# Optimization experiments

Hardware: AMD Instinct MI355X
Metric: run time of the kernel (lower is better)

## Reference

```python
import jax, jax.numpy as jnp
import numpy as np

N_NODES = 100000
N_EDGES = 3200000
NFEAT = 128
NHID = 128


def gcn_conv(x, edge_index, W, b):
    """PyG-style GCNConv: out = D^{-1/2} (A + I) D^{-1/2} (x @ W) + b."""
    n = x.shape[0]
    loop = jnp.arange(n, dtype=edge_index.dtype)
    src = jnp.concatenate([edge_index[0], loop])  # [E + N]
    dst = jnp.concatenate([edge_index[1], loop])  # [E + N]
    # symmetric normalization (degree counted at target, self-loops included)
    deg = jax.ops.segment_sum(jnp.ones_like(dst, dtype=x.dtype), dst, num_segments=n)
    dinv = jnp.where(deg > 0, jax.lax.rsqrt(jnp.maximum(deg, 1.0)), 0.0)
    norm = dinv[src] * dinv[dst]  # [E + N]
    h = x @ W  # [N, F_out] dense projection before aggregation (PyG order)
    msg = h[src] * norm[:, None]  # irregular gather, [E + N, F_out]
    out = jax.ops.segment_sum(msg, dst, num_segments=n)  # scatter-add
    return out + b


def setup_inputs() -> dict:
    key = jax.random.key(0)
    k1, k2, k3, k4 = jax.random.split(key, 4)
    x = jax.random.normal(k1, (N_NODES, NFEAT), dtype=jnp.float32)
    edge_index = jax.random.randint(k2, (2, N_EDGES), 0, N_NODES, dtype=jnp.int64)
    W1 = jax.random.normal(k3, (NFEAT, NHID), dtype=jnp.float32) * 0.05
    b1 = jnp.zeros((NHID,), dtype=jnp.float32)
    W2 = jax.random.normal(k4, (NHID, NHID), dtype=jnp.float32) * 0.05
    b2 = jnp.zeros((NHID,), dtype=jnp.float32)
    return {"x": x, "edge_index": edge_index, "W1": W1, "b1": b1, "W2": W2, "b2": b2}


def reference(x, edge_index, W1, b1, W2, b2):
    # Encoder.forward in eval mode (dropout is identity when training=False)
    h = jax.nn.relu(gcn_conv(x, edge_index, W1, b1))
    h = jax.nn.relu(gcn_conv(h, edge_index, W2, b2))
    return h
```

## Files before the change

kernel.cpp:

```cpp
#include <hip/hip_runtime.h>
#include <hip/hip_fp16.h>
#include <math.h>


#define MB (1u << 20)
#define BCAP 5120
#define EBLK 512

typedef _Float16 f16x8 __attribute__((ext_vector_type(8)));
typedef float f32x4 __attribute__((ext_vector_type(4)));

__global__ __launch_bounds__(256) void k_append(const int* __restrict__ src,
                                                const int* __restrict__ dst,
                                                int* __restrict__ bcnt,
                                                int* __restrict__ staging,
                                                const float* __restrict__ W1,
                                                const float* __restrict__ W2,
                                                _Float16* __restrict__ Wt1,
                                                _Float16* __restrict__ Wt2,
                                                int E, int N, int B) {
  if (blockIdx.x >= EBLK) {
    int idx = (blockIdx.x - EBLK) * 256 + threadIdx.x;
    const float* W = (idx < 16384) ? W1 : W2;
    _Float16* Wt = (idx < 16384) ? Wt1 : Wt2;
    int i = idx & 16383;
    int k = i >> 7, n = i & 127;
    Wt[n * 128 + k] = (_Float16)W[k * 128 + n];
    return;
  }
  __shared__ int lh[1024];
  __shared__ int lb[1024];
  const int t = threadIdx.x;
  const int per = (E + EBLK - 1) / EBLK;
  const int e0 = blockIdx.x * per;
  const int e1 = min(e0 + per, E);

  for (int i = t; i < B; i += 256) lh[i] = 0;
  __syncthreads();
  for (int e = e0 + t; e < e1; e += 256) {
    int d = dst[e], s = src[e];
    if ((unsigned)d < (unsigned)N && (unsigned)s < (unsigned)N)
      atomicAdd(&lh[d >> 7], 1);
  }
  __syncthreads();
  for (int i = t; i < B; i += 256) {
    int c = lh[i];
    lb[i] = c ? atomicAdd(&bcnt[i], c) : 0;
  }
  __syncthreads();
  for (int i = t; i < B; i += 256) lh[i] = 0;
  __syncthreads();
  for (int e = e0 + t; e < e1; e += 256) {
    int d = dst[e], s = src[e];
    if ((unsigned)d < (unsigned)N && (unsigned)s < (unsigned)N) {
      int b = d >> 7;
      int lp = atomicAdd(&lh[b], 1);
      int pos = lb[b] + lp;
      if (pos < BCAP)
        staging[(size_t)b * BCAP + pos] = ((d & 127) << 25) | s;
    }
  }
}

__global__ __launch_bounds__(256) void k_build(const int* __restrict__ staging,
                                               const int* __restrict__ bcnt,
                                               int* __restrict__ rowptr,
                                               float* __restrict__ dinv,
                                               int* __restrict__ col, int N, int B) {
  __shared__ int red[256];
  __shared__ int cnts[128];
  __shared__ int off[128];
  __shared__ int cur[128];
  const int b = blockIdx.x;
  const int t = threadIdx.x;
  const int cnt = min(bcnt[b], BCAP);
  const int* stg = staging + (size_t)b * BCAP;

  int partial = 0;
  for (int i = t; i < b; i += 256) partial += min(bcnt[i], BCAP);
  red[t] = partial;
  if (t < 128) cnts[t] = 0;
  __syncthreads();
  #pragma unroll
  for (int o = 128; o > 0; o >>= 1) {
    if (t < o) red[t] += red[t + o];
    __syncthreads();
  }
  const int ebase = red[0];

  for (int i = t; i < cnt; i += 256)
    atomicAdd(&cnts[((unsigned)stg[i]) >> 25], 1);
  __syncthreads();
  if (t < 128) off[t] = cnts[t];
  __syncthreads();
  for (int d = 1; d < 128; d <<= 1) {
    int v = 0;
    if (t < 128 && t >= d) v = off[t - d];
    __syncthreads();
    if (t < 128) off[t] += v;
    __syncthreads();
  }
  if (t < 128) {
    int node = b * 128 + t;
    if (node < N) {
      int ex = off[t] - cnts[t];
      rowptr[node] = ebase + ex;
      cur[t] = ex;
      dinv[node] = rsqrtf((float)(cnts[t] + 1));
    }
  }
  if (b == B - 1 && t == 0) rowptr[N] = ebase + cnt;
  __syncthreads();
  for (int i = t; i < cnt; i += 256) {
    int p = stg[i];
    int dl = ((unsigned)p) >> 25;
    int s = p & 0x1FFFFFF;
    int lp = atomicAdd(&cur[dl], 1);
    col[ebase + lp] = s;
  }
}

__device__ __forceinline__ void load8(const float* X, size_t base, int kg,
                                      bool relu, _Float16* tmp) {
  float4 v0 = *reinterpret_cast<const float4*>(X + base + kg * 8);
  float4 v1 = *reinterpret_cast<const float4*>(X + base + kg * 8 + 4);
  if (relu) {
    v0.x = fmaxf(v0.x, 0.f); v0.y = fmaxf(v0.y, 0.f);
    v0.z = fmaxf(v0.z, 0.f); v0.w = fmaxf(v0.w, 0.f);
    v1.x = fmaxf(v1.x, 0.f); v1.y = fmaxf(v1.y, 0.f);
    v1.z = fmaxf(v1.z, 0.f); v1.w = fmaxf(v1.w, 0.f);
  }
  tmp[0] = (_Float16)v0.x; tmp[1] = (_Float16)v0.y;
  tmp[2] = (_Float16)v0.z; tmp[3] = (_Float16)v0.w;
  tmp[4] = (_Float16)v1.x; tmp[5] = (_Float16)v1.y;
  tmp[6] = (_Float16)v1.z; tmp[7] = (_Float16)v1.w;
}
__device__ __forceinline__ void load8(const __half* X, size_t base, int kg,
                                      bool relu, _Float16* tmp) {
  uint4 u = *reinterpret_cast<const uint4*>(X + base + kg * 8);
  const _Float16* p = reinterpret_cast<const _Float16*>(&u);
  #pragma unroll
  for (int j = 0; j < 8; j++) {
    _Float16 f = p[j];
    if (relu && (float)f < 0.f) f = (_Float16)0.f;
    tmp[j] = f;
  }
}

template <bool RELU_IN, typename InT>
__global__ __launch_bounds__(256) void k_gemm(const InT* __restrict__ X,
                                              const _Float16* __restrict__ Wt,
                                              const float* __restrict__ dinv,
                                              __half* __restrict__ H, int M) {
  __shared__ __align__(16) _Float16 Xs[64 * 128];
  __shared__ __align__(16) _Float16 Ws[128 * 128];
  const int rb = blockIdx.x * 64;
  const int t = threadIdx.x;

  for (int idx = t; idx < 1024; idx += 256) {
    int row = idx >> 4, kg = idx & 15;
    int grow = rb + row;
    _Float16 tmp[8];
    if (grow < M) {
      load8(X, (size_t)grow * 128, kg, RELU_IN, tmp);
    } else {
      #pragma unroll
      for (int j = 0; j < 8; j++) tmp[j] = (_Float16)0.f;
    }
    int g = kg ^ (row & 7);
    *reinterpret_cast<uint4*>(&Xs[row * 128 + g * 8]) = *reinterpret_cast<uint4*>(tmp);
  }
  for (int idx = t; idx < 2048; idx += 256) {
    int n = idx >> 4, kg = idx & 15;
    uint4 v = *reinterpret_cast<const uint4*>(Wt + n * 128 + kg * 8);
    int g = kg ^ (n & 7);
    *reinterpret_cast<uint4*>(&Ws[n * 128 + g * 8]) = v;
  }
  __syncthreads();

  const int wid = t >> 6;
  const int l = t & 63;
  const int lrow = wid * 16 + (l & 15);
  const int kq = l >> 4;

  f16x8 afrag[4];
  #pragma unroll
  for (int kc = 0; kc < 4; kc++) {
    int kg = kc * 4 + kq;
    int g = kg ^ (lrow & 7);
    afrag[kc] = *reinterpret_cast<const f16x8*>(&Xs[lrow * 128 + g * 8]);
  }
  float dv[4];
  #pragma unroll
  for (int i = 0; i < 4; i++) {
    int grow = rb + wid * 16 + kq * 4 + i;
    dv[i] = (grow < M) ? dinv[grow] : 0.f;
  }

  #pragma unroll 2
  for (int nt = 0; nt < 8; nt++) {
    const int n = nt * 16 + (l & 15);
    f32x4 acc = {};
    #pragma unroll
    for (int kc = 0; kc < 4; kc++) {
      int kg = kc * 4 + kq;
      int g = kg ^ (n & 7);
      f16x8 bfrag = *reinterpret_cast<const f16x8*>(&Ws[n * 128 + g * 8]);
      acc = __builtin_amdgcn_mfma_f32_16x16x32_f16(afrag[kc], bfrag, acc, 0, 0, 0);
    }
    #pragma unroll
    for (int i = 0; i < 4; i++) {
      int grow = rb + wid * 16 + kq * 4 + i;
      if (grow < M)
        H[(size_t)grow * 128 + nt * 16 + (l & 15)] = __float2half(acc[i] * dv[i]);
    }
  }
}

template <bool RELU_OUT, typename OutT>
__global__ __launch_bounds__(256) void k_pull(const __half* __restrict__ hs,
                                              const int* __restrict__ rowptr,
                                              const int* __restrict__ col,
                                              const float* __restrict__ dinv,
                                              const float* __restrict__ bias,
                                              OutT* __restrict__ out, int N) {
  int node = blockIdx.x * 4 + (threadIdx.x >> 6);
  if (node >= N) return;
  node = __builtin_amdgcn_readfirstlane(node);
  const int lane = threadIdx.x & 63;
  const int half = lane >> 5;
  const int fo = (lane & 31) << 2;
  const int start = __builtin_amdgcn_readfirstlane(rowptr[node]);
  const int cnt = __builtin_amdgcn_readfirstlane(rowptr[node + 1]) - start;

  float4 a0 = make_float4(0.f, 0.f, 0.f, 0.f);
  float4 a1 = a0, a2 = a0, a3 = a0;

#define GATHER(sidx, dstacc)                                                   \
  {                                                                            \
    const __half2* p_ =                                                        \
        reinterpret_cast<const __half2*>(hs + (size_t)(sidx) * 128 + fo);      \
    float2 f0_ = __half22float2(p_[0]);                                        \
    float2 f1_ = __half22float2(p_[1]);                                        \
    dstacc.x += f0_.x; dstacc.y += f0_.y;                                      \
    dstacc.z += f1_.x; dstacc.w += f1_.y;                                      \
  }

  int k = 0;
  for (; k + 8 <= cnt; k += 8) {
    int s0 = col[start + k + 0 + half];
    int s1 = col[start + k + 2 + half];
    int s2 = col[start + k + 4 + half];
    int s3 = col[start + k + 6 + half];
    GATHER(s0, a0);
    GATHER(s1, a1);
    GATHER(s2, a2);
    GATHER(s3, a3);
  }
  for (; k + 2 <= cnt; k += 2) {
    int s = col[start + k + half];
    GATHER(s, a0);
  }
  if (k < cnt) {
    int s = col[start + k];
    if (!half) {
      GATHER(s, a1);
    }
  }
#undef GATHER

  float4 acc;
  acc.x = (a0.x + a1.x) + (a2.x + a3.x);
  acc.y = (a0.y + a1.y) + (a2.y + a3.y);
  acc.z = (a0.z + a1.z) + (a2.z + a3.z);
  acc.w = (a0.w + a1.w) + (a2.w + a3.w);
  acc.x += __shfl_xor(acc.x, 32, 64);
  acc.y += __shfl_xor(acc.y, 32, 64);
  acc.z += __shfl_xor(acc.z, 32, 64);
  acc.w += __shfl_xor(acc.w, 32, 64);

  if (!half) {
    const __half2* sp = reinterpret_cast<const __half2*>(hs + (size_t)node * 128 + fo);
    float2 s0 = __half22float2(sp[0]);
    float2 s1 = __half22float2(sp[1]);
    float di = dinv[node];
    float4 bv = *reinterpret_cast<const float4*>(bias + fo);
    float4 o;
    o.x = fmaf(di, acc.x + s0.x, bv.x);
    o.y = fmaf(di, acc.y + s0.y, bv.y);
    o.z = fmaf(di, acc.z + s1.x, bv.z);
    o.w = fmaf(di, acc.w + s1.y, bv.w);
    if (RELU_OUT) {
      o.x = fmaxf(o.x, 0.f); o.y = fmaxf(o.y, 0.f);
      o.z = fmaxf(o.z, 0.f); o.w = fmaxf(o.w, 0.f);
    }
    if constexpr (sizeof(OutT) == 2) {
      __half2 p0 = __float22half2_rn(make_float2(o.x, o.y));
      __half2 p1 = __float22half2_rn(make_float2(o.z, o.w));
      __half2* op = reinterpret_cast<__half2*>((__half*)out + (size_t)node * 128 + fo);
      op[0] = p0;
      op[1] = p1;
    } else {
      *reinterpret_cast<float4*>((float*)out + (size_t)node * 128 + fo) = o;
    }
  }
}

extern "C" void kernel_launch(void* const* d_in, const int* in_sizes, int n_in,
                              void* d_out, int out_size, void* d_ws, size_t ws_size,
                              hipStream_t stream) {
  const float* x  = (const float*)d_in[0];
  const int*   ei = (const int*)d_in[1];
  const float* W1 = (const float*)d_in[2];
  const float* b1 = (const float*)d_in[3];
  const float* W2 = (const float*)d_in[4];
  const float* b2 = (const float*)d_in[5];
  float* out = (float*)d_out;

  const int N = in_sizes[0] / 128;
  const int E = in_sizes[1] / 2;
  const int B = (N + 127) >> 7;
  const int* src = ei;
  const int* dst = ei + E;

  char* ws = (char*)d_ws;
  int*      bcnt    = (int*)     (ws);
  float*    dinv    = (float*)   (ws + 64 * 1024);
  int*      rowptr  = (int*)     (ws + 512 * 1024);
  int*      col     = (int*)     (ws + 1 * MB);
  _Float16* Wt1     = (_Float16*)(ws + 14 * MB - 128 * 1024);
  _Float16* Wt2     = (_Float16*)(ws + 14 * MB - 64 * 1024);
  __half*   h       = (__half*)  (ws + 18 * MB);
  __half*   agg     = (__half*)  (ws + 44 * MB);
  int*      staging = (int*)     (ws + 44 * MB);

  dim3 b256(256);

  hipMemsetAsync(bcnt, 0, (size_t)B * 4, stream);
  k_append<<<EBLK + 128, b256, 0, stream>>>(src, dst, bcnt, staging,
                                            W1, W2, Wt1, Wt2, E, N, B);
  k_build<<<B, b256, 0, stream>>>(staging, bcnt, rowptr, dinv, col, N, B);

  dim3 ggrid((N + 63) / 64);
  dim3 pgrid((N + 3) / 4);

  k_gemm<false, float><<<ggrid, b256, 0, stream>>>(x, Wt1, dinv, h, N);
  k_pull<false, __half><<<pgrid, b256, 0, stream>>>(h, rowptr, col, dinv, b1, agg, N);

  k_gemm<true, __half><<<ggrid, b256, 0, stream>>>(agg, Wt2, dinv, h, N);
  k_pull<true, float><<<pgrid, b256, 0, stream>>>(h, rowptr, col, dinv, b2, out, N);
}
```

Measured before the change: 347.6 us.

## Overlap layer-1 GEMM with edge bucketing and fuse aggregation into layer-2 GEMM

The layer-1 GEMM now writes unscaled features, so it no longer depends on dinv and runs in the same launch as the edge-bucketing blocks. The source-side normalization moves into the gather loop as a per-edge dinv lookup. Layer-1 aggregation, bias and ReLU are fused with the layer-2 GEMM in one 1024-thread kernel, which removes the intermediate agg buffer round trip, the memset and two launches. In exchange, every edge does an extra random dinv load, and the fused kernel makes each wave aggregate four nodes in sequence before the MFMA stage.

```diff
diff --git a/kernel.cpp b/kernel.cpp
--- a/kernel.cpp
+++ b/kernel.cpp
@@ -10,54 +10,133 @@
 typedef _Float16 f16x8 __attribute__((ext_vector_type(8)));
 typedef float f32x4 __attribute__((ext_vector_type(4)));
 
-__global__ __launch_bounds__(256) void k_append(const int* __restrict__ src,
-                                                const int* __restrict__ dst,
-                                                int* __restrict__ bcnt,
-                                                int* __restrict__ staging,
-                                                const float* __restrict__ W1,
-                                                const float* __restrict__ W2,
-                                                _Float16* __restrict__ Wt1,
-                                                _Float16* __restrict__ Wt2,
-                                                int E, int N, int B) {
-  if (blockIdx.x >= EBLK) {
-    int idx = (blockIdx.x - EBLK) * 256 + threadIdx.x;
+__global__ __launch_bounds__(256) void k_init(const float* __restrict__ W1,
+                                              const float* __restrict__ W2,
+                                              _Float16* __restrict__ Wt1,
+                                              _Float16* __restrict__ Wt2,
+                                              int* __restrict__ bcnt, int B) {
+  if (blockIdx.x < 128) {
+    int idx = blockIdx.x * 256 + threadIdx.x;
     const float* W = (idx < 16384) ? W1 : W2;
     _Float16* Wt = (idx < 16384) ? Wt1 : Wt2;
     int i = idx & 16383;
     int k = i >> 7, n = i & 127;
     Wt[n * 128 + k] = (_Float16)W[k * 128 + n];
+  } else {
+    for (int i = threadIdx.x; i < B; i += 256) bcnt[i] = 0;
+  }
+}
+
+union F1Smem {
+  struct { int lh[1024]; int lb[1024]; } a;
+  struct { _Float16 Xs[64 * 128]; _Float16 Ws[128 * 128]; } g;
+};
+
+__global__ __launch_bounds__(256) void k_f1(const float* __restrict__ X,
+                                            const _Float16* __restrict__ Wt1,
+                                            __half* __restrict__ H, int M, int GB,
+                                            const int* __restrict__ src,
+                                            const int* __restrict__ dst,
+                                            int* __restrict__ bcnt,
+                                            int* __restrict__ staging,
+                                            int E, int N, int B) {
+  __shared__ __align__(16) F1Smem sm;
+  const int t = threadIdx.x;
+
+  if ((int)blockIdx.x >= GB) {
+    int* lh = sm.a.lh;
+    int* lb = sm.a.lb;
+    const int bid = blockIdx.x - GB;
+    const int per = (E + EBLK - 1) / EBLK;
+    const int e0 = bid * per;
+    const int e1 = min(e0 + per, E);
+
+    for (int i = t; i < B; i += 256) lh[i] = 0;
+    __syncthreads();
+    for (int e = e0 + t; e < e1; e += 256) {
+      int d = dst[e], s = src[e];
+      if ((unsigned)d < (unsigned)N && (unsigned)s < (unsigned)N)
+        atomicAdd(&lh[d >> 7], 1);
+    }
+    __syncthreads();
+    for (int i = t; i < B; i += 256) {
+      int c = lh[i];
+      lb[i] = c ? atomicAdd(&bcnt[i], c) : 0;
+    }
+    __syncthreads();
+    for (int i = t; i < B; i += 256) lh[i] = 0;
+    __syncthreads();
+    for (int e = e0 + t; e < e1; e += 256) {
+      int d = dst[e], s = src[e];
+      if ((unsigned)d < (unsigned)N && (unsigned)s < (unsigned)N) {
+        int b = d >> 7;
+        int lp = atomicAdd(&lh[b], 1);
+        int pos = lb[b] + lp;
+        if (pos < BCAP)
+          staging[(size_t)b * BCAP + pos] = ((d & 127) << 25) | s;
+      }
+    }
     return;
   }
-  __shared__ int lh[1024];
-  __shared__ int lb[1024];
-  const int t = threadIdx.x;
-  const int per = (E + EBLK - 1) / EBLK;
-  const int e0 = blockIdx.x * per;
-  const int e1 = min(e0 + per, E);
-
-  for (int i = t; i < B; i += 256) lh[i] = 0;
-  __syncthreads();
-  for (int e = e0 + t; e < e1; e += 256) {
-    int d = dst[e], s = src[e];
-    if ((unsigned)d < (unsigned)N && (unsigned)s < (unsigned)N)
-      atomicAdd(&lh[d >> 7], 1);
-  }
-  __syncthreads();
-  for (int i = t; i < B; i += 256) {
-    int c = lh[i];
-    lb[i] = c ? atomicAdd(&bcnt[i], c) : 0;
-  }
-  __syncthreads();
-  for (int i = t; i < B; i += 256) lh[i] = 0;
-  __syncthreads();
-  for (int e = e0 + t; e < e1; e += 256) {
-    int d = dst[e], s = src[e];
-    if ((unsigned)d < (unsigned)N && (unsigned)s < (unsigned)N) {
-      int b = d >> 7;
-      int lp = atomicAdd(&lh[b], 1);
-      int pos = lb[b] + lp;
-      if (pos < BCAP)
-        staging[(size_t)b * BCAP + pos] = ((d & 127) << 25) | s;
+
+  _Float16* Xs = sm.g.Xs;
+  _Float16* Ws = sm.g.Ws;
+  const int rb = blockIdx.x * 64;
+
+  for (int idx = t; idx < 1024; idx += 256) {
+    int row = idx >> 4, kg = idx & 15;
+    int grow = rb + row;
+    _Float16 tmp[8];
+    if (grow < M) {
+      float4 v0 = *reinterpret_cast<const float4*>(X + (size_t)grow * 128 + kg * 8);
+      float4 v1 = *reinterpret_cast<const float4*>(X + (size_t)grow * 128 + kg * 8 + 4);
+      tmp[0] = (_Float16)v0.x; tmp[1] = (_Float16)v0.y;
+      tmp[2] = (_Float16)v0.z; tmp[3] = (_Float16)v0.w;
+      tmp[4] = (_Float16)v1.x; tmp[5] = (_Float16)v1.y;
+      tmp[6] = (_Float16)v1.z; tmp[7] = (_Float16)v1.w;
+    } else {
+      #pragma unroll
+      for (int j = 0; j < 8; j++) tmp[j] = (_Float16)0.f;
+    }
+    int g = kg ^ (row & 7);
+    *reinterpret_cast<uint4*>(&Xs[row * 128 + g * 8]) = *reinterpret_cast<uint4*>(tmp);
+  }
+  for (int idx = t; idx < 2048; idx += 256) {
+    int n = idx >> 4, kg = idx & 15;
+    uint4 v = *reinterpret_cast<const uint4*>(Wt1 + n * 128 + kg * 8);
+    int g = kg ^ (n & 7);
+    *reinterpret_cast<uint4*>(&Ws[n * 128 + g * 8]) = v;
+  }
+  __syncthreads();
+
+  const int wid = t >> 6;
+  const int l = t & 63;
+  const int lrow = wid * 16 + (l & 15);
+  const int kq = l >> 4;
+
+  f16x8 afrag[4];
+  #pragma unroll
+  for (int kc = 0; kc < 4; kc++) {
+    int kg = kc * 4 + kq;
+    int g = kg ^ (lrow & 7);
+    afrag[kc] = *reinterpret_cast<const f16x8*>(&Xs[lrow * 128 + g * 8]);
+  }
+  #pragma unroll 2
+  for (int nt = 0; nt < 8; nt++) {
+    const int n = nt * 16 + (l & 15);
+    f32x4 acc = {};
+    #pragma unroll
+    for (int kc = 0; kc < 4; kc++) {
+      int kg = kc * 4 + kq;
+      int g = kg ^ (n & 7);
+      f16x8 bfrag = *reinterpret_cast<const f16x8*>(&Ws[n * 128 + g * 8]);
+      acc = __builtin_amdgcn_mfma_f32_16x16x32_f16(afrag[kc], bfrag, acc, 0, 0, 0);
+    }
+    #pragma unroll
+    for (int i = 0; i < 4; i++) {
+      int grow = rb + wid * 16 + kq * 4 + i;
+      if (grow < M)
+        H[(size_t)grow * 128 + nt * 16 + (l & 15)] = __float2half(acc[i]);
     }
   }
 }
@@ -120,69 +199,83 @@
   }
 }
 
-__device__ __forceinline__ void load8(const float* X, size_t base, int kg,
-                                      bool relu, _Float16* tmp) {
-  float4 v0 = *reinterpret_cast<const float4*>(X + base + kg * 8);
-  float4 v1 = *reinterpret_cast<const float4*>(X + base + kg * 8 + 4);
-  if (relu) {
-    v0.x = fmaxf(v0.x, 0.f); v0.y = fmaxf(v0.y, 0.f);
-    v0.z = fmaxf(v0.z, 0.f); v0.w = fmaxf(v0.w, 0.f);
-    v1.x = fmaxf(v1.x, 0.f); v1.y = fmaxf(v1.y, 0.f);
-    v1.z = fmaxf(v1.z, 0.f); v1.w = fmaxf(v1.w, 0.f);
-  }
-  tmp[0] = (_Float16)v0.x; tmp[1] = (_Float16)v0.y;
-  tmp[2] = (_Float16)v0.z; tmp[3] = (_Float16)v0.w;
-  tmp[4] = (_Float16)v1.x; tmp[5] = (_Float16)v1.y;
-  tmp[6] = (_Float16)v1.z; tmp[7] = (_Float16)v1.w;
-}
-__device__ __forceinline__ void load8(const __half* X, size_t base, int kg,
-                                      bool relu, _Float16* tmp) {
-  uint4 u = *reinterpret_cast<const uint4*>(X + base + kg * 8);
-  const _Float16* p = reinterpret_cast<const _Float16*>(&u);
-  #pragma unroll
-  for (int j = 0; j < 8; j++) {
-    _Float16 f = p[j];
-    if (relu && (float)f < 0.f) f = (_Float16)0.f;
-    tmp[j] = f;
-  }
-}
-
-template <bool RELU_IN, typename InT>
-__global__ __launch_bounds__(256) void k_gemm(const InT* __restrict__ X,
-                                              const _Float16* __restrict__ Wt,
-                                              const float* __restrict__ dinv,
-                                              __half* __restrict__ H, int M) {
+__device__ __forceinline__ float2 gather_row_sum(const __half* __restrict__ hs,
+                                                 const int* __restrict__ col,
+                                                 const float* __restrict__ dinv,
+                                                 int start, int cnt, int lane) {
+  const __half2* h2 = reinterpret_cast<const __half2*>(hs);
+  float ax0 = 0.f, ay0 = 0.f, ax1 = 0.f, ay1 = 0.f;
+  float ax2 = 0.f, ay2 = 0.f, ax3 = 0.f, ay3 = 0.f;
+  int k = 0;
+  for (; k + 4 <= cnt; k += 4) {
+    int s0 = col[start + k + 0];
+    int s1 = col[start + k + 1];
+    int s2 = col[start + k + 2];
+    int s3 = col[start + k + 3];
+    float d0 = dinv[s0], d1 = dinv[s1], d2 = dinv[s2], d3 = dinv[s3];
+    float2 v0 = __half22float2(h2[(size_t)s0 * 64 + lane]);
+    float2 v1 = __half22float2(h2[(size_t)s1 * 64 + lane]);
+    float2 v2 = __half22float2(h2[(size_t)s2 * 64 + lane]);
+    float2 v3 = __half22float2(h2[(size_t)s3 * 64 + lane]);
+    ax0 = fmaf(v0.x, d0, ax0); ay0 = fmaf(v0.y, d0, ay0);
+    ax1 = fmaf(v1.x, d1, ax1); ay1 = fmaf(v1.y, d1, ay1);
+    ax2 = fmaf(v2.x, d2, ax2); ay2 = fmaf(v2.y, d2, ay2);
+    ax3 = fmaf(v3.x, d3, ax3); ay3 = fmaf(v3.y, d3, ay3);
+  }
+  for (; k < cnt; k++) {
+    int s = col[start + k];
+    float d = dinv[s];
+    float2 v = __half22float2(h2[(size_t)s * 64 + lane]);
+    ax0 = fmaf(v.x, d, ax0); ay0 = fmaf(v.y, d, ay0);
+  }
+  return make_float2((ax0 + ax1) + (ax2 + ax3), (ay0 + ay1) + (ay2 + ay3));
+}
+
+__global__ __launch_bounds__(1024) void k_pullgemm(const __half* __restrict__ hs,
+                                                   const int* __restrict__ rowptr,
+                                                   const int* __restrict__ col,
+                                                   const float* __restrict__ dinv,
+                                                   const float* __restrict__ b1,
+                                                   const _Float16* __restrict__ Wt2,
+                                                   __half* __restrict__ H2, int N) {
   __shared__ __align__(16) _Float16 Xs[64 * 128];
   __shared__ __align__(16) _Float16 Ws[128 * 128];
-  const int rb = blockIdx.x * 64;
   const int t = threadIdx.x;
-
-  for (int idx = t; idx < 1024; idx += 256) {
-    int row = idx >> 4, kg = idx & 15;
-    int grow = rb + row;
-    _Float16 tmp[8];
-    if (grow < M) {
-      load8(X, (size_t)grow * 128, kg, RELU_IN, tmp);
-    } else {
-      #pragma unroll
-      for (int j = 0; j < 8; j++) tmp[j] = (_Float16)0.f;
-    }
-    int g = kg ^ (row & 7);
-    *reinterpret_cast<uint4*>(&Xs[row * 128 + g * 8]) = *reinterpret_cast<uint4*>(tmp);
-  }
-  for (int idx = t; idx < 2048; idx += 256) {
+  const int nb = blockIdx.x * 64;
+
+  for (int idx = t; idx < 2048; idx += 1024) {
     int n = idx >> 4, kg = idx & 15;
-    uint4 v = *reinterpret_cast<const uint4*>(Wt + n * 128 + kg * 8);
+    uint4 v = *reinterpret_cast<const uint4*>(Wt2 + n * 128 + kg * 8);
     int g = kg ^ (n & 7);
     *reinterpret_cast<uint4*>(&Ws[n * 128 + g * 8]) = v;
   }
-  __syncthreads();
-
-  const int wid = t >> 6;
-  const int l = t & 63;
-  const int lrow = wid * 16 + (l & 15);
-  const int kq = l >> 4;
-
+
+  const int w = t >> 6, lane = t & 63;
+  const __half2* h2 = reinterpret_cast<const __half2*>(hs);
+
+  for (int rep = 0; rep < 4; rep++) {
+    const int r = w * 4 + rep;
+    const int node = nb + r;
+    float2 o = make_float2(0.f, 0.f);
+    if (node < N) {
+      const int start = __builtin_amdgcn_readfirstlane(rowptr[node]);
+      const int cnt = __builtin_amdgcn_readfirstlane(rowptr[node + 1]) - start;
+      float2 acc = gather_row_sum(hs, col, dinv, start, cnt, lane);
+      float di = dinv[node];
+      float2 self = __half22float2(h2[(size_t)node * 64 + lane]);
+      float2 bv = reinterpret_cast<const float2*>(b1)[lane];
+      o.x = fmaxf(fmaf(di, fmaf(self.x, di, acc.x), bv.x), 0.f);
+      o.y = fmaxf(fmaf(di, fmaf(self.y, di, acc.y), bv.y), 0.f);
+    }
+    int kg = lane >> 2;
+    int off = (lane & 3) * 2;
+    __half2 oh = __float22half2_rn(o);
+    *reinterpret_cast<__half2*>(&Xs[r * 128 + (kg ^ (r & 7)) * 8 + off]) = oh;
+  }
+  __syncthreads();
+
+  const int lrow = (w & 3) * 16 + (lane & 15);
+  const int kq = lane >> 4;
   f16x8 afrag[4];
   #pragma unroll
   for (int kc = 0; kc < 4; kc++) {
@@ -190,16 +283,10 @@
     int g = kg ^ (lrow & 7);
     afrag[kc] = *reinterpret_cast<const f16x8*>(&Xs[lrow * 128 + g * 8]);
   }
-  float dv[4];
   #pragma unroll
-  for (int i = 0; i < 4; i++) {
-    int grow = rb + wid * 16 + kq * 4 + i;
-    dv[i] = (grow < M) ? dinv[grow] : 0.f;
-  }
-
-  #pragma unroll 2
-  for (int nt = 0; nt < 8; nt++) {
-    const int n = nt * 16 + (l & 15);
+  for (int q = 0; q < 2; q++) {
+    int nt = (w >> 2) * 2 + q;
+    int n = nt * 16 + (lane & 15);
     f32x4 acc = {};
     #pragma unroll
     for (int kc = 0; kc < 4; kc++) {
@@ -210,100 +297,34 @@
     }
     #pragma unroll
     for (int i = 0; i < 4; i++) {
-      int grow = rb + wid * 16 + kq * 4 + i;
-      if (grow < M)
-        H[(size_t)grow * 128 + nt * 16 + (l & 15)] = __float2half(acc[i] * dv[i]);
-    }
-  }
-}
-
-template <bool RELU_OUT, typename OutT>
-__global__ __launch_bounds__(256) void k_pull(const __half* __restrict__ hs,
-                                              const int* __restrict__ rowptr,
-                                              const int* __restrict__ col,
-                                              const float* __restrict__ dinv,
-                                              const float* __restrict__ bias,
-                                              OutT* __restrict__ out, int N) {
+      int grow = nb + (w & 3) * 16 + kq * 4 + i;
+      if (grow < N)
+        H2[(size_t)grow * 128 + nt * 16 + (lane & 15)] = __float2half(acc[i]);
+    }
+  }
+}
+
+__global__ __launch_bounds__(256) void k_pull2(const __half* __restrict__ hs,
+                                               const int* __restrict__ rowptr,
+                                               const int* __restrict__ col,
+                                               const float* __restrict__ dinv,
+                                               const float* __restrict__ bias,
+                                               float* __restrict__ out, int N) {
   int node = blockIdx.x * 4 + (threadIdx.x >> 6);
   if (node >= N) return;
   node = __builtin_amdgcn_readfirstlane(node);
   const int lane = threadIdx.x & 63;
-  const int half = lane >> 5;
-  const int fo = (lane & 31) << 2;
   const int start = __builtin_amdgcn_readfirstlane(rowptr[node]);
   const int cnt = __builtin_amdgcn_readfirstlane(rowptr[node + 1]) - start;
-
-  float4 a0 = make_float4(0.f, 0.f, 0.f, 0.f);
-  float4 a1 = a0, a2 = a0, a3 = a0;
-
-#define GATHER(sidx, dstacc)                                                   \
-  {                                                                            \
-    const __half2* p_ =                                                        \
-        reinterpret_cast<const __half2*>(hs + (size_t)(sidx) * 128 + fo);      \
-    float2 f0_ = __half22float2(p_[0]);                                        \
-    float2 f1_ = __half22float2(p_[1]);                                        \
-    dstacc.x += f0_.x; dstacc.y += f0_.y;                                      \
-    dstacc.z += f1_.x; dstacc.w += f1_.y;                                      \
-  }
-
-  int k = 0;
-  for (; k + 8 <= cnt; k += 8) {
-    int s0 = col[start + k + 0 + half];
-    int s1 = col[start + k + 2 + half];
-    int s2 = col[start + k + 4 + half];
-    int s3 = col[start + k + 6 + half];
-    GATHER(s0, a0);
-    GATHER(s1, a1);
-    GATHER(s2, a2);
-    GATHER(s3, a3);
-  }
-  for (; k + 2 <= cnt; k += 2) {
-    int s = col[start + k + half];
-    GATHER(s, a0);
-  }
-  if (k < cnt) {
-    int s = col[start + k];
-    if (!half) {
-      GATHER(s, a1);
-    }
-  }
-#undef GATHER
-
-  float4 acc;
-  acc.x = (a0.x + a1.x) + (a2.x + a3.x);
-  acc.y = (a0.y + a1.y) + (a2.y + a3.y);
-  acc.z = (a0.z + a1.z) + (a2.z + a3.z);
-  acc.w = (a0.w + a1.w) + (a2.w + a3.w);
-  acc.x += __shfl_xor(acc.x, 32, 64);
-  acc.y += __shfl_xor(acc.y, 32, 64);
-  acc.z += __shfl_xor(acc.z, 32, 64);
-  acc.w += __shfl_xor(acc.w, 32, 64);
-
-  if (!half) {
-    const __half2* sp = reinterpret_cast<const __half2*>(hs + (size_t)node * 128 + fo);
-    float2 s0 = __half22float2(sp[0]);
-    float2 s1 = __half22float2(sp[1]);
-    float di = dinv[node];
-    float4 bv = *reinterpret_cast<const float4*>(bias + fo);
-    float4 o;
-    o.x = fmaf(di, acc.x + s0.x, bv.x);
-    o.y = fmaf(di, acc.y + s0.y, bv.y);
-    o.z = fmaf(di, acc.z + s1.x, bv.z);
-    o.w = fmaf(di, acc.w + s1.y, bv.w);
-    if (RELU_OUT) {
-      o.x = fmaxf(o.x, 0.f); o.y = fmaxf(o.y, 0.f);
-      o.z = fmaxf(o.z, 0.f); o.w = fmaxf(o.w, 0.f);
-    }
-    if constexpr (sizeof(OutT) == 2) {
-      __half2 p0 = __float22half2_rn(make_float2(o.x, o.y));
-      __half2 p1 = __float22half2_rn(make_float2(o.z, o.w));
-      __half2* op = reinterpret_cast<__half2*>((__half*)out + (size_t)node * 128 + fo);
-      op[0] = p0;
-      op[1] = p1;
-    } else {
-      *reinterpret_cast<float4*>((float*)out + (size_t)node * 128 + fo) = o;
-    }
-  }
+  float2 acc = gather_row_sum(hs, col, dinv, start, cnt, lane);
+  float di = dinv[node];
+  float2 self = __half22float2(
+      reinterpret_cast<const __half2*>(hs)[(size_t)node * 64 + lane]);
+  float2 bv = reinterpret_cast<const float2*>(bias)[lane];
+  float2 o;
+  o.x = fmaxf(fmaf(di, fmaf(self.x, di, acc.x), bv.x), 0.f);
+  o.y = fmaxf(fmaf(di, fmaf(self.y, di, acc.y), bv.y), 0.f);
+  reinterpret_cast<float2*>(out)[(size_t)node * 64 + lane] = o;
 }
 
 extern "C" void kernel_launch(void* const* d_in, const int* in_sizes, int n_in,
@@ -320,6 +341,7 @@
   const int N = in_sizes[0] / 128;
   const int E = in_sizes[1] / 2;
   const int B = (N + 127) >> 7;
+  const int GB = (N + 63) / 64;
   const int* src = ei;
   const int* dst = ei + E;
 
@@ -331,22 +353,15 @@
   _Float16* Wt1     = (_Float16*)(ws + 14 * MB - 128 * 1024);
   _Float16* Wt2     = (_Float16*)(ws + 14 * MB - 64 * 1024);
   __half*   h       = (__half*)  (ws + 18 * MB);
-  __half*   agg     = (__half*)  (ws + 44 * MB);
   int*      staging = (int*)     (ws + 44 * MB);
+  __half*   h2      = (__half*)  (ws + 44 * MB);
 
   dim3 b256(256);
 
-  hipMemsetAsync(bcnt, 0, (size_t)B * 4, stream);
-  k_append<<<EBLK + 128, b256, 0, stream>>>(src, dst, bcnt, staging,
-                                            W1, W2, Wt1, Wt2, E, N, B);
+  k_init<<<129, b256, 0, stream>>>(W1, W2, Wt1, Wt2, bcnt, B);
+  k_f1<<<GB + EBLK, b256, 0, stream>>>(x, Wt1, h, N, GB, src, dst, bcnt,
+                                       staging, E, N, B);
   k_build<<<B, b256, 0, stream>>>(staging, bcnt, rowptr, dinv, col, N, B);
-
-  dim3 ggrid((N + 63) / 64);
-  dim3 pgrid((N + 3) / 4);
-
-  k_gemm<false, float><<<ggrid, b256, 0, stream>>>(x, Wt1, dinv, h, N);
-  k_pull<false, __half><<<pgrid, b256, 0, stream>>>(h, rowptr, col, dinv, b1, agg, N);
-
-  k_gemm<true, __half><<<ggrid, b256, 0, stream>>>(agg, Wt2, dinv, h, N);
-  k_pull<true, float><<<pgrid, b256, 0, stream>>>(h, rowptr, col, dinv, b2, out, N);
-}
+  k_pullgemm<<<GB, dim3(1024), 0, stream>>>(h, rowptr, col, dinv, b1, Wt2, h2, N);
+  k_pull2<<<(N + 3) / 4, b256, 0, stream>>>(h2, rowptr, col, dinv, b2, out, N);
+}
```

New measurement: 353.7 us. Within noise of the previous version (+1.8%).

## Fuse first GEMM with edge bucketing and move source normalization into gather

Applied to the files above, without the earlier changes.

The first projection X@W1 no longer depends on the degree normalization, because dinv[src] is now applied per edge inside the gather. That lets the GEMM run in the same launch as the edge-bucketing blocks, so the dense work overlaps the atomic-heavy append phase. The memset and weight transpose move into a small init kernel, and the ReLU on the layer-1 output moves into the pull epilogue, which removes it from the second GEMM's load. The cost is an extra dinv load per gathered edge, and the staging area no longer aliases agg, so the workspace layout changes.

```diff
diff --git a/kernel.cpp b/kernel.cpp
--- a/kernel.cpp
+++ b/kernel.cpp
@@ -10,54 +10,133 @@
 typedef _Float16 f16x8 __attribute__((ext_vector_type(8)));
 typedef float f32x4 __attribute__((ext_vector_type(4)));
 
-__global__ __launch_bounds__(256) void k_append(const int* __restrict__ src,
-                                                const int* __restrict__ dst,
-                                                int* __restrict__ bcnt,
-                                                int* __restrict__ staging,
-                                                const float* __restrict__ W1,
-                                                const float* __restrict__ W2,
-                                                _Float16* __restrict__ Wt1,
-                                                _Float16* __restrict__ Wt2,
-                                                int E, int N, int B) {
-  if (blockIdx.x >= EBLK) {
-    int idx = (blockIdx.x - EBLK) * 256 + threadIdx.x;
+__global__ __launch_bounds__(256) void k_init(const float* __restrict__ W1,
+                                              const float* __restrict__ W2,
+                                              _Float16* __restrict__ Wt1,
+                                              _Float16* __restrict__ Wt2,
+                                              int* __restrict__ bcnt, int B) {
+  if (blockIdx.x < 128) {
+    int idx = blockIdx.x * 256 + threadIdx.x;
     const float* W = (idx < 16384) ? W1 : W2;
     _Float16* Wt = (idx < 16384) ? Wt1 : Wt2;
     int i = idx & 16383;
     int k = i >> 7, n = i & 127;
     Wt[n * 128 + k] = (_Float16)W[k * 128 + n];
+  } else {
+    for (int i = threadIdx.x; i < B; i += 256) bcnt[i] = 0;
+  }
+}
+
+union F1Smem {
+  struct { int lh[1024]; int lb[1024]; } a;
+  struct { _Float16 Xs[64 * 128]; _Float16 Ws[128 * 128]; } g;
+};
+
+__global__ __launch_bounds__(256) void k_f1(const float* __restrict__ X,
+                                            const _Float16* __restrict__ Wt1,
+                                            __half* __restrict__ H, int M, int GB,
+                                            const int* __restrict__ src,
+                                            const int* __restrict__ dst,
+                                            int* __restrict__ bcnt,
+                                            int* __restrict__ staging,
+                                            int E, int N, int B) {
+  __shared__ __align__(16) F1Smem sm;
+  const int t = threadIdx.x;
+
+  if ((int)blockIdx.x >= GB) {
+    int* lh = sm.a.lh;
+    int* lb = sm.a.lb;
+    const int bid = blockIdx.x - GB;
+    const int per = (E + EBLK - 1) / EBLK;
+    const int e0 = bid * per;
+    const int e1 = min(e0 + per, E);
+
+    for (int i = t; i < B; i += 256) lh[i] = 0;
+    __syncthreads();
+    for (int e = e0 + t; e < e1; e += 256) {
+      int d = dst[e], s = src[e];
+      if ((unsigned)d < (unsigned)N && (unsigned)s < (unsigned)N)
+        atomicAdd(&lh[d >> 7], 1);
+    }
+    __syncthreads();
+    for (int i = t; i < B; i += 256) {
+      int c = lh[i];
+      lb[i] = c ? atomicAdd(&bcnt[i], c) : 0;
+    }
+    __syncthreads();
+    for (int i = t; i < B; i += 256) lh[i] = 0;
+    __syncthreads();
+    for (int e = e0 + t; e < e1; e += 256) {
+      int d = dst[e], s = src[e];
+      if ((unsigned)d < (unsigned)N && (unsigned)s < (unsigned)N) {
+        int b = d >> 7;
+        int lp = atomicAdd(&lh[b], 1);
+        int pos = lb[b] + lp;
+        if (pos < BCAP)
+          staging[(size_t)b * BCAP + pos] = ((d & 127) << 25) | s;
+      }
+    }
     return;
   }
-  __shared__ int lh[1024];
-  __shared__ int lb[1024];
-  const int t = threadIdx.x;
-  const int per = (E + EBLK - 1) / EBLK;
-  const int e0 = blockIdx.x * per;
-  const int e1 = min(e0 + per, E);
-
-  for (int i = t; i < B; i += 256) lh[i] = 0;
-  __syncthreads();
-  for (int e = e0 + t; e < e1; e += 256) {
-    int d = dst[e], s = src[e];
-    if ((unsigned)d < (unsigned)N && (unsigned)s < (unsigned)N)
-      atomicAdd(&lh[d >> 7], 1);
-  }
-  __syncthreads();
-  for (int i = t; i < B; i += 256) {
-    int c = lh[i];
-    lb[i] = c ? atomicAdd(&bcnt[i], c) : 0;
-  }
-  __syncthreads();
-  for (int i = t; i < B; i += 256) lh[i] = 0;
-  __syncthreads();
-  for (int e = e0 + t; e < e1; e += 256) {
-    int d = dst[e], s = src[e];
-    if ((unsigned)d < (unsigned)N && (unsigned)s < (unsigned)N) {
-      int b = d >> 7;
-      int lp = atomicAdd(&lh[b], 1);
-      int pos = lb[b] + lp;
-      if (pos < BCAP)
-        staging[(size_t)b * BCAP + pos] = ((d & 127) << 25) | s;
+
+  _Float16* Xs = sm.g.Xs;
+  _Float16* Ws = sm.g.Ws;
+  const int rb = blockIdx.x * 64;
+
+  for (int idx = t; idx < 1024; idx += 256) {
+    int row = idx >> 4, kg = idx & 15;
+    int grow = rb + row;
+    _Float16 tmp[8];
+    if (grow < M) {
+      float4 v0 = *reinterpret_cast<const float4*>(X + (size_t)grow * 128 + kg * 8);
+      float4 v1 = *reinterpret_cast<const float4*>(X + (size_t)grow * 128 + kg * 8 + 4);
+      tmp[0] = (_Float16)v0.x; tmp[1] = (_Float16)v0.y;
+      tmp[2] = (_Float16)v0.z; tmp[3] = (_Float16)v0.w;
+      tmp[4] = (_Float16)v1.x; tmp[5] = (_Float16)v1.y;
+      tmp[6] = (_Float16)v1.z; tmp[7] = (_Float16)v1.w;
+    } else {
+      #pragma unroll
+      for (int j = 0; j < 8; j++) tmp[j] = (_Float16)0.f;
+    }
+    int g = kg ^ (row & 7);
+    *reinterpret_cast<uint4*>(&Xs[row * 128 + g * 8]) = *reinterpret_cast<uint4*>(tmp);
+  }
+  for (int idx = t; idx < 2048; idx += 256) {
+    int n = idx >> 4, kg = idx & 15;
+    uint4 v = *reinterpret_cast<const uint4*>(Wt1 + n * 128 + kg * 8);
+    int g = kg ^ (n & 7);
+    *reinterpret_cast<uint4*>(&Ws[n * 128 + g * 8]) = v;
+  }
+  __syncthreads();
+
+  const int wid = t >> 6;
+  const int l = t & 63;
+  const int lrow = wid * 16 + (l & 15);
+  const int kq = l >> 4;
+
+  f16x8 afrag[4];
+  #pragma unroll
+  for (int kc = 0; kc < 4; kc++) {
+    int kg = kc * 4 + kq;
+    int g = kg ^ (lrow & 7);
+    afrag[kc] = *reinterpret_cast<const f16x8*>(&Xs[lrow * 128 + g * 8]);
+  }
+  #pragma unroll 2
+  for (int nt = 0; nt < 8; nt++) {
+    const int n = nt * 16 + (l & 15);
+    f32x4 acc = {};
+    #pragma unroll
+    for (int kc = 0; kc < 4; kc++) {
+      int kg = kc * 4 + kq;
+      int g = kg ^ (n & 7);
+      f16x8 bfrag = *reinterpret_cast<const f16x8*>(&Ws[n * 128 + g * 8]);
+      acc = __builtin_amdgcn_mfma_f32_16x16x32_f16(afrag[kc], bfrag, acc, 0, 0, 0);
+    }
+    #pragma unroll
+    for (int i = 0; i < 4; i++) {
+      int grow = rb + wid * 16 + kq * 4 + i;
+      if (grow < M)
+        H[(size_t)grow * 128 + nt * 16 + (l & 15)] = __float2half(acc[i]);
     }
   }
 }
@@ -120,37 +199,8 @@
   }
 }
 
-__device__ __forceinline__ void load8(const float* X, size_t base, int kg,
-                                      bool relu, _Float16* tmp) {
-  float4 v0 = *reinterpret_cast<const float4*>(X + base + kg * 8);
-  float4 v1 = *reinterpret_cast<const float4*>(X + base + kg * 8 + 4);
-  if (relu) {
-    v0.x = fmaxf(v0.x, 0.f); v0.y = fmaxf(v0.y, 0.f);
-    v0.z = fmaxf(v0.z, 0.f); v0.w = fmaxf(v0.w, 0.f);
-    v1.x = fmaxf(v1.x, 0.f); v1.y = fmaxf(v1.y, 0.f);
-    v1.z = fmaxf(v1.z, 0.f); v1.w = fmaxf(v1.w, 0.f);
-  }
-  tmp[0] = (_Float16)v0.x; tmp[1] = (_Float16)v0.y;
-  tmp[2] = (_Float16)v0.z; tmp[3] = (_Float16)v0.w;
-  tmp[4] = (_Float16)v1.x; tmp[5] = (_Float16)v1.y;
-  tmp[6] = (_Float16)v1.z; tmp[7] = (_Float16)v1.w;
-}
-__device__ __forceinline__ void load8(const __half* X, size_t base, int kg,
-                                      bool relu, _Float16* tmp) {
-  uint4 u = *reinterpret_cast<const uint4*>(X + base + kg * 8);
-  const _Float16* p = reinterpret_cast<const _Float16*>(&u);
-  #pragma unroll
-  for (int j = 0; j < 8; j++) {
-    _Float16 f = p[j];
-    if (relu && (float)f < 0.f) f = (_Float16)0.f;
-    tmp[j] = f;
-  }
-}
-
-template <bool RELU_IN, typename InT>
-__global__ __launch_bounds__(256) void k_gemm(const InT* __restrict__ X,
+__global__ __launch_bounds__(256) void k_gemm(const __half* __restrict__ X,
                                               const _Float16* __restrict__ Wt,
-                                              const float* __restrict__ dinv,
                                               __half* __restrict__ H, int M) {
   __shared__ __align__(16) _Float16 Xs[64 * 128];
   __shared__ __align__(16) _Float16 Ws[128 * 128];
@@ -160,15 +210,11 @@
   for (int idx = t; idx < 1024; idx += 256) {
     int row = idx >> 4, kg = idx & 15;
     int grow = rb + row;
-    _Float16 tmp[8];
-    if (grow < M) {
-      load8(X, (size_t)grow * 128, kg, RELU_IN, tmp);
-    } else {
-      #pragma unroll
-      for (int j = 0; j < 8; j++) tmp[j] = (_Float16)0.f;
-    }
+    uint4 v = make_uint4(0, 0, 0, 0);
+    if (grow < M)
+      v = *reinterpret_cast<const uint4*>(X + (size_t)grow * 128 + kg * 8);
     int g = kg ^ (row & 7);
-    *reinterpret_cast<uint4*>(&Xs[row * 128 + g * 8]) = *reinterpret_cast<uint4*>(tmp);
+    *reinterpret_cast<uint4*>(&Xs[row * 128 + g * 8]) = v;
   }
   for (int idx = t; idx < 2048; idx += 256) {
     int n = idx >> 4, kg = idx & 15;
@@ -190,13 +236,6 @@
     int g = kg ^ (lrow & 7);
     afrag[kc] = *reinterpret_cast<const f16x8*>(&Xs[lrow * 128 + g * 8]);
   }
-  float dv[4];
-  #pragma unroll
-  for (int i = 0; i < 4; i++) {
-    int grow = rb + wid * 16 + kq * 4 + i;
-    dv[i] = (grow < M) ? dinv[grow] : 0.f;
-  }
-
   #pragma unroll 2
   for (int nt = 0; nt < 8; nt++) {
     const int n = nt * 16 + (l & 15);
@@ -212,12 +251,12 @@
     for (int i = 0; i < 4; i++) {
       int grow = rb + wid * 16 + kq * 4 + i;
       if (grow < M)
-        H[(size_t)grow * 128 + nt * 16 + (l & 15)] = __float2half(acc[i] * dv[i]);
-    }
-  }
-}
-
-template <bool RELU_OUT, typename OutT>
+        H[(size_t)grow * 128 + nt * 16 + (l & 15)] = __float2half(acc[i]);
+    }
+  }
+}
+
+template <typename OutT>
 __global__ __launch_bounds__(256) void k_pull(const __half* __restrict__ hs,
                                               const int* __restrict__ rowptr,
                                               const int* __restrict__ col,
@@ -238,12 +277,15 @@
 
 #define GATHER(sidx, dstacc)                                                   \
   {                                                                            \
+    float d_ = dinv[sidx];                                                     \
     const __half2* p_ =                                                        \
         reinterpret_cast<const __half2*>(hs + (size_t)(sidx) * 128 + fo);      \
     float2 f0_ = __half22float2(p_[0]);                                        \
     float2 f1_ = __half22float2(p_[1]);                                        \
-    dstacc.x += f0_.x; dstacc.y += f0_.y;                                      \
-    dstacc.z += f1_.x; dstacc.w += f1_.y;                                      \
+    dstacc.x = fmaf(f0_.x, d_, dstacc.x);                                      \
+    dstacc.y = fmaf(f0_.y, d_, dstacc.y);                                      \
+    dstacc.z = fmaf(f1_.x, d_, dstacc.z);                                      \
+    dstacc.w = fmaf(f1_.y, d_, dstacc.w);                                      \
   }
 
   int k = 0;
@@ -286,14 +328,10 @@
     float di = dinv[node];
     float4 bv = *reinterpret_cast<const float4*>(bias + fo);
     float4 o;
-    o.x = fmaf(di, acc.x + s0.x, bv.x);
-    o.y = fmaf(di, acc.y + s0.y, bv.y);
-    o.z = fmaf(di, acc.z + s1.x, bv.z);
-    o.w = fmaf(di, acc.w + s1.y, bv.w);
-    if (RELU_OUT) {
-      o.x = fmaxf(o.x, 0.f); o.y = fmaxf(o.y, 0.f);
-      o.z = fmaxf(o.z, 0.f); o.w = fmaxf(o.w, 0.f);
-    }
+    o.x = fmaxf(fmaf(di, fmaf(di, s0.x, acc.x), bv.x), 0.f);
+    o.y = fmaxf(fmaf(di, fmaf(di, s0.y, acc.y), bv.y), 0.f);
+    o.z = fmaxf(fmaf(di, fmaf(di, s1.x, acc.z), bv.z), 0.f);
+    o.w = fmaxf(fmaf(di, fmaf(di, s1.y, acc.w), bv.w), 0.f);
     if constexpr (sizeof(OutT) == 2) {
       __half2 p0 = __float22half2_rn(make_float2(o.x, o.y));
       __half2 p1 = __float22half2_rn(make_float2(o.z, o.w));
@@ -320,6 +358,7 @@
   const int N = in_sizes[0] / 128;
   const int E = in_sizes[1] / 2;
   const int B = (N + 127) >> 7;
+  const int GB = (N + 63) / 64;
   const int* src = ei;
   const int* dst = ei + E;
 
@@ -331,22 +370,16 @@
   _Float16* Wt1     = (_Float16*)(ws + 14 * MB - 128 * 1024);
   _Float16* Wt2     = (_Float16*)(ws + 14 * MB - 64 * 1024);
   __half*   h       = (__half*)  (ws + 18 * MB);
-  __half*   agg     = (__half*)  (ws + 44 * MB);
   int*      staging = (int*)     (ws + 44 * MB);
+  __half*   agg     = (__half*)  (ws + 60 * MB);
 
   dim3 b256(256);
 
-  hipMemsetAsync(bcnt, 0, (size_t)B * 4, stream);
-  k_append<<<EBLK + 128, b256, 0, stream>>>(src, dst, bcnt, staging,
-                                            W1, W2, Wt1, Wt2, E, N, B);
+  k_init<<<129, b256, 0, stream>>>(W1, W2, Wt1, Wt2, bcnt, B);
+  k_f1<<<GB + EBLK, b256, 0, stream>>>(x, Wt1, h, N, GB, src, dst, bcnt,
+                                       staging, E, N, B);
   k_build<<<B, b256, 0, stream>>>(staging, bcnt, rowptr, dinv, col, N, B);
-
-  dim3 ggrid((N + 63) / 64);
-  dim3 pgrid((N + 3) / 4);
-
-  k_gemm<false, float><<<ggrid, b256, 0, stream>>>(x, Wt1, dinv, h, N);
-  k_pull<false, __half><<<pgrid, b256, 0, stream>>>(h, rowptr, col, dinv, b1, agg, N);
-
-  k_gemm<true, __half><<<ggrid, b256, 0, stream>>>(agg, Wt2, dinv, h, N);
-  k_pull<true, float><<<pgrid, b256, 0, stream>>>(h, rowptr, col, dinv, b2, out, N);
-}
+  k_pull<__half><<<(N + 3) / 4, b256, 0, stream>>>(h, rowptr, col, dinv, b1, agg, N);
+  k_gemm<<<GB, b256, 0, stream>>>(agg, Wt2, h, N);
+  k_pull<float><<<(N + 3) / 4, b256, 0, stream>>>(h, rowptr, col, dinv, b2, out, N);
+}
```

New measurement: 346.8 us. No clear change (-0.2%).
